# Kernel optimization log

Measured on AMD Instinct MI355X. Metric: run time of the kernel, lower is better.

## Reference

```python
import jax, jax.numpy as jnp
import numpy as np

B, S, D, H = 2, 2048, 1024, 16
HD = D // H
EPS = 1e-5


def setup_inputs() -> dict:
    key = jax.random.key(0)
    ks = jax.random.split(key, 12)
    s = 1.0 / np.sqrt(D)
    inp = {
        "q": jax.random.normal(ks[0], (B, S, D), jnp.float32),
        "k": jax.random.normal(ks[1], (B, S, D), jnp.float32),
        "v": jax.random.normal(ks[2], (B, S, D), jnp.float32),
        "mask": jnp.ones((B, S, S), jnp.int32),
        "Wq": jax.random.normal(ks[3], (D, D), jnp.float32) * s,
        "bq": jnp.zeros((D,), jnp.float32),
        "Wk": jax.random.normal(ks[4], (D, D), jnp.float32) * s,
        "bk": jnp.zeros((D,), jnp.float32),
        "Wv": jax.random.normal(ks[5], (D, D), jnp.float32) * s,
        "bv": jnp.zeros((D,), jnp.float32),
        "Wo": jax.random.normal(ks[6], (D, D), jnp.float32) * s,
        "bo": jnp.zeros((D,), jnp.float32),
        "gamma": jnp.ones((D,), jnp.float32),
        "beta": jnp.zeros((D,), jnp.float32),
    }
    return inp


def reference(q, k, v, mask, Wq, bq, Wk, bk, Wv, bv, Wo, bo, gamma, beta):
    residual = q
    # projections (torch Linear: x @ W.T + b)
    qh = (q @ Wq.T + bq).reshape(B, S, H, HD).transpose(0, 2, 1, 3)  # b h s d
    kh = (k @ Wk.T + bk).reshape(B, S, H, HD).transpose(0, 2, 1, 3)
    vh = (v @ Wv.T + bv).reshape(B, S, H, HD).transpose(0, 2, 1, 3)
    scores = jnp.einsum('bhid,bhjd->bhij', qh, kh) / jnp.sqrt(jnp.float32(HD))
    scores = jnp.where(mask[:, None, :, :] == 0, jnp.float32(-1e9), scores)
    attention = jax.nn.softmax(scores, axis=-1)  # dropout=0 (eval)
    context = jnp.einsum('bhij,bhjd->bhid', attention, vh)
    context = context.transpose(0, 2, 1, 3).reshape(B, S, D)
    out = context @ Wo.T + bo
    x = out + residual
    mu = jnp.mean(x, axis=-1, keepdims=True)
    var = jnp.mean(jnp.square(x - mu), axis=-1, keepdims=True)
    output = (x - mu) * jax.lax.rsqrt(var + EPS) * gamma + beta
    return (output, attention)
```

## Files before the change

### kernel.cpp

```cpp
#include <hip/hip_runtime.h>
#include <hip/hip_bf16.h>


typedef float f32x4 __attribute__((ext_vector_type(4)));
typedef short short8 __attribute__((ext_vector_type(8)));

#if __has_builtin(__builtin_amdgcn_exp2f)
#define EXP2(x) __builtin_amdgcn_exp2f(x)
#else
#define EXP2(x) exp2f(x)
#endif

#define QSCALE 0.18033688011112042f
#define MASKNEG -1.4426950408889634e9f

#define BAR_DRAIN8()  asm volatile("s_waitcnt vmcnt(8) lgkmcnt(0)\ns_barrier" ::: "memory")
#define BAR_LGKM()    asm volatile("s_waitcnt lgkmcnt(0)\ns_barrier" ::: "memory")

__device__ __forceinline__ short f2bs(float f) {
  union { __hip_bfloat16 h; short s; } u;
  u.h = __float2bfloat16(f);
  return u.s;
}

__device__ __forceinline__ void async16(const void* g, void* l) {
  __builtin_amdgcn_global_load_lds(
      (const __attribute__((address_space(1))) unsigned int*)g,
      (__attribute__((address_space(3))) unsigned int*)l, 16, 0, 0);
}

__global__ __launch_bounds__(256) void cvt_mask_kernel(
    const float* __restrict__ q, const float* __restrict__ k, const float* __restrict__ v,
    const float* __restrict__ wq, const float* __restrict__ wk, const float* __restrict__ wv,
    const float* __restrict__ wo, short* __restrict__ dst,
    const int* __restrict__ mask, unsigned* __restrict__ bits, unsigned* __restrict__ flags) {
  if (blockIdx.x < 8192) {
    long base = (long)blockIdx.x * 2048;
    const float* src;
    if      (base <  4194304) src = q  + base;
    else if (base <  8388608) src = k  + (base - 4194304);
    else if (base < 12582912) src = v  + (base - 8388608);
    else if (base < 13631488) src = wq + (base - 12582912);
    else if (base < 14680064) src = wk + (base - 13631488);
    else if (base < 15728640) src = wv + (base - 14680064);
    else                      src = wo + (base - 15728640);
    int off = threadIdx.x * 8;
    float4 a = *(const float4*)(src + off);
    float4 b = *(const float4*)(src + off + 4);
    short8 o;
    o[0] = f2bs(a.x); o[1] = f2bs(a.y); o[2] = f2bs(a.z); o[3] = f2bs(a.w);
    o[4] = f2bs(b.x); o[5] = f2bs(b.y); o[6] = f2bs(b.z); o[7] = f2bs(b.w);
    *(short8*)(dst + base + off) = o;
  } else {
    int bid = blockIdx.x - 8192;
    int t = threadIdx.x, w = t >> 6, lane = t & 63;
    for (int it = 0; it < 16; ++it) {
      long gw = (long)it * 8192 + bid * 4 + w;
      long base = gw * 64;
      int mv = mask[base + lane];
      unsigned long long m = __ballot(mv != 0);
      if (lane == 0)  bits[gw * 2]     = (unsigned)m;
      if (lane == 32) bits[gw * 2 + 1] = (unsigned)(m >> 32);
      if (lane == 0 && m != 0xFFFFFFFFFFFFFFFFull) {
        long j = base & 2047, i = (base >> 11) & 2047, b = base >> 22;
        atomicOr(&flags[(int)(b * 256 + (i >> 7) * 16 + (j >> 7))], 1u);
      }
    }
  }
}

__global__ __launch_bounds__(256, 2) void proj_kernel(
    const short* __restrict__ Abase, const short* __restrict__ Wbase,
    const float* __restrict__ bq, const float* __restrict__ bk, const float* __restrict__ bv,
    short* __restrict__ Qh, short* __restrict__ Kh, short* __restrict__ Vt) {
  __shared__ __align__(16) short As[2][128 * 64];
  __shared__ __align__(16) short Bs[2][128 * 64];
  const int mode = blockIdx.z;
  const short* A = Abase + (size_t)mode * 4194304;
  const short* W = Wbase + (size_t)mode * 1048576;
  const float* bias = (mode == 0) ? bq : (mode == 1 ? bk : bv);
  const int t = threadIdx.x, w = t >> 6, lane = t & 63, g = lane >> 4, lc = lane & 15;
  const int wrow = (w >> 1) * 64, wcol = (w & 1) * 64;
  const int m0 = blockIdx.x * 128, n0 = blockIdx.y * 128;

#define PSTAGE(buf, k0)                                                                     \
  do {                                                                                      \
    _Pragma("unroll") for (int i_ = 0; i_ < 4; i_++) {                                      \
      int cb = i_ * 256 + w * 64, ch = cb + lane, row = ch >> 3, c = ch & 7;                \
      int so = ((c ^ (row & 7)) << 3);                                                      \
      async16(A + (size_t)(m0 + row) * 1024 + (k0) + so, (void*)&As[buf][cb << 3]);         \
      async16(W + (size_t)(n0 + row) * 1024 + (k0) + so, (void*)&Bs[buf][cb << 3]);         \
    }                                                                                       \
  } while (0)

  f32x4 acc[4][4] = {};
  PSTAGE(0, 0);
  __syncthreads();
  int pb = 0;
  for (int kt = 0; kt < 16; ++kt) {
    if (kt < 15) PSTAGE(pb ^ 1, (kt + 1) * 64);
#pragma unroll
    for (int kf = 0; kf < 2; ++kf) {
      short8 af[4], bf[4];
#pragma unroll
      for (int m = 0; m < 4; m++) {
        int row = wrow + m * 16 + lc;
        af[m] = *(const short8*)&As[pb][(row << 6) + (((kf * 4 + g) ^ (row & 7)) << 3)];
      }
#pragma unroll
      for (int n = 0; n < 4; n++) {
        int row = wcol + n * 16 + lc;
        bf[n] = *(const short8*)&Bs[pb][(row << 6) + (((kf * 4 + g) ^ (row & 7)) << 3)];
      }
      __builtin_amdgcn_s_setprio(1);
#pragma unroll
      for (int m = 0; m < 4; m++)
#pragma unroll
        for (int n = 0; n < 4; n++)
          acc[m][n] = __builtin_amdgcn_mfma_f32_16x16x32_bf16(af[m], bf[n], acc[m][n], 0, 0, 0);
      __builtin_amdgcn_s_setprio(0);
    }
    __syncthreads();
    pb ^= 1;
  }
#undef PSTAGE
#pragma unroll
  for (int n = 0; n < 4; n++) {
    const int col = n0 + wcol + n * 16 + lc;
    const float bv_ = bias[col];
    const int h = col >> 6, d = col & 63;
#pragma unroll
    for (int m = 0; m < 4; m++)
#pragma unroll
      for (int r = 0; r < 4; r++) {
        const int srow = m0 + wrow + m * 16 + g * 4 + r;
        const int b = srow >> 11, s = srow & 2047;
        float val = acc[m][n][r] + bv_;
        if (mode == 0)
          Qh[((size_t)(b * 16 + h) * 2048 + s) * 64 + d] = f2bs(val * QSCALE);
        else if (mode == 1)
          Kh[((size_t)(b * 16 + h) * 2048 + s) * 64 + d] = f2bs(val);
        else
          Vt[((size_t)(b * 16 + h) * 64 + d) * 2048 + s] = f2bs(val);
      }
  }
}

__global__ __launch_bounds__(512, 4) void attn_kernel(
    const short* __restrict__ Qh, const short* __restrict__ Kh, const short* __restrict__ Vt,
    const unsigned* __restrict__ mbits, const unsigned* __restrict__ mflags,
    float* __restrict__ Pout, short* __restrict__ ctx) {
  __shared__ __align__(16) short Ks[2][128 * 64];
  __shared__ __align__(16) short Vs[64 * 128];
  __shared__ __align__(16) short Ps[128 * 128];
  const int L = blockIdx.x;
  const int xcd = L & 7, idx = L >> 3;
  const int bh = xcd + ((idx >> 4) << 3);
  const int qb = idx & 15;
  const int b = bh >> 4, h = bh & 15;
  const int t = threadIdx.x, w = t >> 6, lane = t & 63, g = lane >> 4, lc = lane & 15;
  const short* Qp = Qh + (size_t)bh * 2048 * 64;
  const short* Kp = Kh + (size_t)bh * 2048 * 64;
  const short* Vp = Vt + (size_t)bh * 64 * 2048;
  float* Pb = Pout + ((size_t)bh * 2048 + qb * 128) * 2048;

  short8 qf[2];
#pragma unroll
  for (int kf = 0; kf < 2; kf++)
    qf[kf] = *(const short8*)(Qp + (size_t)(qb * 128 + w * 16 + lc) * 64 + kf * 32 + g * 8);

#define STAGE_K(buf, j0)                                                                   \
  do {                                                                                     \
    _Pragma("unroll") for (int i_ = 0; i_ < 2; i_++) {                                     \
      int cb = i_ * 512 + w * 64, ch = cb + lane, row = ch >> 3, c = ch & 7;               \
      int sc = c ^ (row & 7) ^ ((row >> 3) & 7);                                           \
      async16(Kp + (size_t)((j0) + row) * 64 + (sc << 3), (void*)&Ks[buf][cb << 3]);       \
    }                                                                                      \
  } while (0)
#define STAGE_V(j0)                                                                        \
  do {                                                                                     \
    _Pragma("unroll") for (int i_ = 0; i_ < 2; i_++) {                                     \
      int cb = i_ * 512 + w * 64, ch = cb + lane, row = ch >> 4, c = ch & 15;              \
      async16(Vp + (size_t)row * 2048 + (j0) + ((c ^ (row & 15)) << 3), (void*)&Vs[cb << 3]); \
    }                                                                                      \
  } while (0)

  float lsum = 0.f;
  int kb = 0;
  STAGE_K(0, 0);
  __syncthreads();
  for (int it = 0; it < 16; ++it) {
    if (it < 15) STAGE_K(kb ^ 1, (it + 1) * 128);
    f32x4 acc[8] = {};
    __builtin_amdgcn_s_setprio(1);
#pragma unroll
    for (int kf = 0; kf < 2; kf++)
#pragma unroll
      for (int n = 0; n < 8; n++) {
        int row = n * 16 + lc;
        int sc = (kf * 4 + g) ^ (row & 7) ^ ((row >> 3) & 7);
        short8 kfr = *(const short8*)&Ks[kb][(row << 6) + (sc << 3)];
        acc[n] = __builtin_amdgcn_mfma_f32_16x16x32_bf16(kfr, qf[kf], acc[n], 0, 0, 0);
      }
    __builtin_amdgcn_s_setprio(0);
    unsigned flg = mflags[b * 256 + qb * 16 + it];
    if (flg) {
      int ig = qb * 128 + w * 16 + lc;
      uint4 mw = *(const uint4*)(mbits + ((size_t)b * 2048 + ig) * 64 + it * 4);
#pragma unroll
      for (int n = 0; n < 8; n++) {
        unsigned bw = (n >> 1) == 0 ? mw.x : ((n >> 1) == 1 ? mw.y : ((n >> 1) == 2 ? mw.z : mw.w));
#pragma unroll
        for (int r = 0; r < 4; r++)
          if (!((bw >> (((n & 1) << 4) + g * 4 + r)) & 1u)) acc[n][r] = MASKNEG;
      }
    }
    float s_ = 0.f;
#pragma unroll
    for (int n = 0; n < 8; n++)
#pragma unroll
      for (int r = 0; r < 4; r++) s_ += EXP2(acc[n][r]);
    s_ += __shfl_xor(s_, 16);
    s_ += __shfl_xor(s_, 32);
    lsum += s_;
    __syncthreads();
    kb ^= 1;
  }
  float* ls = (float*)Vs;
  if (g == 0) ls[w * 16 + lc] = lsum;
  __syncthreads();
  float linv[4];
#pragma unroll
  for (int r = 0; r < 4; r++) linv[r] = 1.0f / ls[w * 16 + g * 4 + r];
  kb = 0;
  STAGE_K(0, 0);
  __syncthreads();

  f32x4 acco[4] = {};
  for (int it = 0; it < 16; ++it) {
    const int j0 = it * 128;
    STAGE_V(j0);
    if (it < 15) STAGE_K(kb ^ 1, j0 + 128);
    f32x4 accs[8] = {};
    __builtin_amdgcn_s_setprio(1);
#pragma unroll
    for (int kf = 0; kf < 2; kf++)
#pragma unroll
      for (int n = 0; n < 8; n++) {
        int row = lc * 8 + n;
        int sc = (kf * 4 + g) ^ n ^ (lc & 7);
        short8 kfr = *(const short8*)&Ks[kb][(row << 6) + (sc << 3)];
        accs[n] = __builtin_amdgcn_mfma_f32_16x16x32_bf16(qf[kf], kfr, accs[n], 0, 0, 0);
      }
    __builtin_amdgcn_s_setprio(0);
    unsigned flg = mflags[b * 256 + qb * 16 + it];
    if (flg) {
#pragma unroll
      for (int r = 0; r < 4; r++) {
        int ig = qb * 128 + w * 16 + g * 4 + r;
        uint4 mw = *(const uint4*)(mbits + ((size_t)b * 2048 + ig) * 64 + it * 4);
        unsigned w01 = (lc & 4) ? mw.y : mw.x;
        unsigned w23 = (lc & 4) ? mw.w : mw.z;
        unsigned wsel = (lc & 8) ? w23 : w01;
#pragma unroll
        for (int n = 0; n < 8; n++)
          if (!((wsel >> (((lc & 3) << 3) + n)) & 1u)) accs[n][r] = MASKNEG;
      }
    }
#pragma unroll
    for (int r = 0; r < 4; r++) {
      const float li = linv[r];
      const int irow = w * 16 + g * 4 + r;
      f32x4 p0, p1;
#pragma unroll
      for (int n = 0; n < 4; n++) p0[n] = EXP2(accs[n][r]) * li;
#pragma unroll
      for (int n = 0; n < 4; n++) p1[n] = EXP2(accs[n + 4][r]) * li;
      float* pr = Pb + (size_t)irow * 2048 + j0 + (lc << 3);
      *(f32x4*)pr = p0;
      *(f32x4*)(pr + 4) = p1;
      short8 pk;
#pragma unroll
      for (int n = 0; n < 4; n++) { pk[n] = f2bs(p0[n]); pk[n + 4] = f2bs(p1[n]); }
      *(short8*)&Ps[(irow << 7) + ((lc ^ (irow & 15)) << 3)] = pk;
    }
    BAR_DRAIN8();
    __builtin_amdgcn_s_setprio(1);
#pragma unroll
    for (int kt4 = 0; kt4 < 4; kt4++) {
      int prow = w * 16 + lc;
      short8 pa = *(const short8*)&Ps[(prow << 7) + ((((kt4 << 2) + g) ^ (prow & 15)) << 3)];
#pragma unroll
      for (int dn = 0; dn < 4; dn++) {
        int d = dn * 16 + lc;
        short8 vb_ = *(const short8*)&Vs[(d << 7) + ((((kt4 << 2) + g) ^ (d & 15)) << 3)];
        acco[dn] = __builtin_amdgcn_mfma_f32_16x16x32_bf16(pa, vb_, acco[dn], 0, 0, 0);
      }
    }
    __builtin_amdgcn_s_setprio(0);
    BAR_LGKM();
    kb ^= 1;
  }
#pragma unroll
  for (int dn = 0; dn < 4; dn++)
#pragma unroll
    for (int r = 0; r < 4; r++) {
      int srow = qb * 128 + w * 16 + g * 4 + r;
      int col = h * 64 + dn * 16 + lc;
      ctx[(size_t)(b * 2048 + srow) * 1024 + col] = f2bs(acco[dn][r]);
    }
#undef STAGE_K
#undef STAGE_V
}

__global__ __launch_bounds__(256, 2) void oproj_kernel(
    const short* __restrict__ A, const short* __restrict__ W,
    const float* __restrict__ bo, const float* __restrict__ qres, float* __restrict__ xo) {
  __shared__ __align__(16) short As[2][128 * 64];
  __shared__ __align__(16) short Bs[2][128 * 64];
  const int t = threadIdx.x, w = t >> 6, lane = t & 63, g = lane >> 4, lc = lane & 15;
  const int wrow = (w >> 1) * 64, wcol = (w & 1) * 64;
  const int m0 = blockIdx.x * 128, n0 = blockIdx.y * 128;

#define OSTAGE(buf, k0)                                                                     \
  do {                                                                                      \
    _Pragma("unroll") for (int i_ = 0; i_ < 4; i_++) {                                      \
      int cb = i_ * 256 + w * 64, ch = cb + lane, row = ch >> 3, c = ch & 7;                \
      int so = ((c ^ (row & 7)) << 3);                                                      \
      async16(A + (size_t)(m0 + row) * 1024 + (k0) + so, (void*)&As[buf][cb << 3]);         \
      async16(W + (size_t)(n0 + row) * 1024 + (k0) + so, (void*)&Bs[buf][cb << 3]);         \
    }                                                                                       \
  } while (0)

  f32x4 acc[4][4] = {};
  OSTAGE(0, 0);
  __syncthreads();
  int pb = 0;
  for (int kt = 0; kt < 16; ++kt) {
    if (kt < 15) OSTAGE(pb ^ 1, (kt + 1) * 64);
#pragma unroll
    for (int kf = 0; kf < 2; ++kf) {
      short8 af[4], bf[4];
#pragma unroll
      for (int m = 0; m < 4; m++) {
        int row = wrow + m * 16 + lc;
        af[m] = *(const short8*)&As[pb][(row << 6) + (((kf * 4 + g) ^ (row & 7)) << 3)];
      }
#pragma unroll
      for (int n = 0; n < 4; n++) {
        int row = wcol + n * 16 + lc;
        bf[n] = *(const short8*)&Bs[pb][(row << 6) + (((kf * 4 + g) ^ (row & 7)) << 3)];
      }
      __builtin_amdgcn_s_setprio(1);
#pragma unroll
      for (int m = 0; m < 4; m++)
#pragma unroll
        for (int n = 0; n < 4; n++)
          acc[m][n] = __builtin_amdgcn_mfma_f32_16x16x32_bf16(af[m], bf[n], acc[m][n], 0, 0, 0);
      __builtin_amdgcn_s_setprio(0);
    }
    __syncthreads();
    pb ^= 1;
  }
#undef OSTAGE
#pragma unroll
  for (int n = 0; n < 4; n++) {
    const int col = n0 + wcol + n * 16 + lc;
    const float bv_ = bo[col];
#pragma unroll
    for (int m = 0; m < 4; m++)
#pragma unroll
      for (int r = 0; r < 4; r++) {
        const int srow = m0 + wrow + m * 16 + g * 4 + r;
        size_t o = (size_t)srow * 1024 + col;
        xo[o] = acc[m][n][r] + bv_ + qres[o];
      }
  }
}

__global__ __launch_bounds__(256) void ln_kernel(const float* __restrict__ x,
                                                 const float* __restrict__ gamma,
                                                 const float* __restrict__ beta,
                                                 float* __restrict__ out) {
  const int row = blockIdx.x, t = threadIdx.x;
  const float4 v = ((const float4*)(x + (size_t)row * 1024))[t];
  float s = v.x + v.y + v.z + v.w;
  float sq = v.x * v.x + v.y * v.y + v.z * v.z + v.w * v.w;
#pragma unroll
  for (int off = 1; off < 64; off <<= 1) { s += __shfl_xor(s, off); sq += __shfl_xor(sq, off); }
  __shared__ float ss[4], sqs[4];
  const int w = t >> 6, lane = t & 63;
  if (lane == 0) { ss[w] = s; sqs[w] = sq; }
  __syncthreads();
  s = ss[0] + ss[1] + ss[2] + ss[3];
  sq = sqs[0] + sqs[1] + sqs[2] + sqs[3];
  const float mu = s * (1.f / 1024.f);
  const float var = sq * (1.f / 1024.f) - mu * mu;
  const float rs = rsqrtf(var + 1e-5f);
  const float4 gm = ((const float4*)gamma)[t];
  const float4 bt = ((const float4*)beta)[t];
  float4 o;
  o.x = (v.x - mu) * rs * gm.x + bt.x;
  o.y = (v.y - mu) * rs * gm.y + bt.y;
  o.z = (v.z - mu) * rs * gm.z + bt.z;
  o.w = (v.w - mu) * rs * gm.w + bt.w;
  ((float4*)(out + (size_t)row * 1024))[t] = o;
}

extern "C" void kernel_launch(void* const* d_in, const int* in_sizes, int n_in,
                              void* d_out, int out_size, void* d_ws, size_t ws_size,
                              hipStream_t stream) {
  (void)in_sizes; (void)n_in; (void)out_size; (void)ws_size;
  const float* q     = (const float*)d_in[0];
  const float* k     = (const float*)d_in[1];
  const float* v     = (const float*)d_in[2];
  const int*   mask  = (const int*)d_in[3];
  const float* Wq    = (const float*)d_in[4];
  const float* bq    = (const float*)d_in[5];
  const float* Wk    = (const float*)d_in[6];
  const float* bk    = (const float*)d_in[7];
  const float* Wv    = (const float*)d_in[8];
  const float* bv    = (const float*)d_in[9];
  const float* Wo    = (const float*)d_in[10];
  const float* bo    = (const float*)d_in[11];
  const float* gamma = (const float*)d_in[12];
  const float* beta  = (const float*)d_in[13];

  char* ws = (char*)d_ws;
  short* cvtdst = (short*)ws;
  short* Qh     = (short*)(ws + 33554432);
  short* Kh     = (short*)(ws + 41943040);
  short* Vt     = (short*)(ws + 50331648);
  unsigned* mbits  = (unsigned*)(ws + 58720256);
  unsigned* mflags = (unsigned*)(ws + 59768832);
  float* x   = (float*)ws;
  short* ctx = (short*)(ws + 16777216);

  float* outln = (float*)d_out;
  float* Pout  = (float*)d_out + 4194304;

  hipMemsetAsync(mflags, 0, 2048, stream);
  cvt_mask_kernel<<<10240, 256, 0, stream>>>(q, k, v, Wq, Wk, Wv, Wo, cvtdst, mask, mbits, mflags);
  proj_kernel<<<dim3(32, 8, 3), 256, 0, stream>>>(cvtdst, cvtdst + 12582912, bq, bk, bv, Qh, Kh, Vt);
  attn_kernel<<<512, 512, 0, stream>>>(Qh, Kh, Vt, mbits, mflags, Pout, ctx);
  oproj_kernel<<<dim3(32, 8), 256, 0, stream>>>(ctx, cvtdst + 15728640, bo, q, x);
  ln_kernel<<<4096, 256, 0, stream>>>(x, gamma, beta, outln);
}
```

Measured before the change: 285.3 us.

## Deepen K prefetch in attention row-sum pass with five-slot LDS ring

Merges the attention kernel's separate K, V and P shared buffers into one five-slot LDS array. The first pass, which computes the softmax row sums, now prefetches two K tiles ahead and handles two tiles per barrier pair, cutting barriers and exposing less load latency. The second pass changes its vmcnt waits so the prefetched K load can stay in flight past the P-V barrier. This adds fragile hand-counted waitcnt values, and an error in those counts would cause races.

```diff
diff --git a/kernel.cpp b/kernel.cpp
--- a/kernel.cpp
+++ b/kernel.cpp
@@ -13,9 +13,6 @@
 
 #define QSCALE 0.18033688011112042f
 #define MASKNEG -1.4426950408889634e9f
-
-#define BAR_DRAIN8()  asm volatile("s_waitcnt vmcnt(8) lgkmcnt(0)\ns_barrier" ::: "memory")
-#define BAR_LGKM()    asm volatile("s_waitcnt lgkmcnt(0)\ns_barrier" ::: "memory")
 
 __device__ __forceinline__ short f2bs(float f) {
   union { __hip_bfloat16 h; short s; } u;
@@ -150,9 +147,7 @@
     const short* __restrict__ Qh, const short* __restrict__ Kh, const short* __restrict__ Vt,
     const unsigned* __restrict__ mbits, const unsigned* __restrict__ mflags,
     float* __restrict__ Pout, short* __restrict__ ctx) {
-  __shared__ __align__(16) short Ks[2][128 * 64];
-  __shared__ __align__(16) short Vs[64 * 128];
-  __shared__ __align__(16) short Ps[128 * 128];
+  __shared__ __align__(16) short SH[5][8192];
   const int L = blockIdx.x;
   const int xcd = L & 7, idx = L >> 3;
   const int bh = xcd + ((idx >> 4) << 3);
@@ -169,78 +164,88 @@
   for (int kf = 0; kf < 2; kf++)
     qf[kf] = *(const short8*)(Qp + (size_t)(qb * 128 + w * 16 + lc) * 64 + kf * 32 + g * 8);
 
-#define STAGE_K(buf, j0)                                                                   \
+#define STAGE_KS(dst, tj)                                                                  \
   do {                                                                                     \
     _Pragma("unroll") for (int i_ = 0; i_ < 2; i_++) {                                     \
       int cb = i_ * 512 + w * 64, ch = cb + lane, row = ch >> 3, c = ch & 7;               \
       int sc = c ^ (row & 7) ^ ((row >> 3) & 7);                                           \
-      async16(Kp + (size_t)((j0) + row) * 64 + (sc << 3), (void*)&Ks[buf][cb << 3]);       \
+      async16(Kp + (size_t)((tj) * 128 + row) * 64 + (sc << 3), (void*)&(dst)[cb << 3]);   \
     }                                                                                      \
   } while (0)
 #define STAGE_V(j0)                                                                        \
   do {                                                                                     \
     _Pragma("unroll") for (int i_ = 0; i_ < 2; i_++) {                                     \
       int cb = i_ * 512 + w * 64, ch = cb + lane, row = ch >> 4, c = ch & 15;              \
-      async16(Vp + (size_t)row * 2048 + (j0) + ((c ^ (row & 15)) << 3), (void*)&Vs[cb << 3]); \
+      async16(Vp + (size_t)row * 2048 + (j0) + ((c ^ (row & 15)) << 3), (void*)&SH[2][cb << 3]); \
     }                                                                                      \
   } while (0)
 
   float lsum = 0.f;
+  STAGE_KS((&SH[0][0]), 0);
+  STAGE_KS((&SH[1][0]), 1);
+  for (int p = 0; p < 8; ++p) {
+    asm volatile("s_waitcnt lgkmcnt(0)\ns_barrier" ::: "memory");
+    if (p < 7) {
+      STAGE_KS((&SH[(2 * p + 2) % 5][0]), 2 * p + 2);
+      STAGE_KS((&SH[(2 * p + 3) % 5][0]), 2 * p + 3);
+    }
+    if (p < 7) asm volatile("s_waitcnt vmcnt(4)\ns_barrier" ::: "memory");
+    else       asm volatile("s_waitcnt vmcnt(0)\ns_barrier" ::: "memory");
+#pragma unroll
+    for (int half = 0; half < 2; ++half) {
+      const int it = 2 * p + half;
+      const short* Kslot = &SH[it % 5][0];
+      f32x4 acc[8] = {};
+      __builtin_amdgcn_s_setprio(1);
+#pragma unroll
+      for (int kf = 0; kf < 2; kf++)
+#pragma unroll
+        for (int n = 0; n < 8; n++) {
+          int row = n * 16 + lc;
+          int sc = (kf * 4 + g) ^ (row & 7) ^ ((row >> 3) & 7);
+          short8 kfr = *(const short8*)&Kslot[(row << 6) + (sc << 3)];
+          acc[n] = __builtin_amdgcn_mfma_f32_16x16x32_bf16(kfr, qf[kf], acc[n], 0, 0, 0);
+        }
+      __builtin_amdgcn_s_setprio(0);
+      unsigned flg = mflags[b * 256 + qb * 16 + it];
+      if (flg) {
+        int ig = qb * 128 + w * 16 + lc;
+        uint4 mw = *(const uint4*)(mbits + ((size_t)b * 2048 + ig) * 64 + it * 4);
+#pragma unroll
+        for (int n = 0; n < 8; n++) {
+          unsigned bw = (n >> 1) == 0 ? mw.x : ((n >> 1) == 1 ? mw.y : ((n >> 1) == 2 ? mw.z : mw.w));
+#pragma unroll
+          for (int r = 0; r < 4; r++)
+            if (!((bw >> (((n & 1) << 4) + g * 4 + r)) & 1u)) acc[n][r] = MASKNEG;
+        }
+      }
+      float s_ = 0.f;
+#pragma unroll
+      for (int n = 0; n < 8; n++)
+#pragma unroll
+        for (int r = 0; r < 4; r++) s_ += EXP2(acc[n][r]);
+      s_ += __shfl_xor(s_, 16);
+      s_ += __shfl_xor(s_, 32);
+      lsum += s_;
+    }
+  }
+  float* ls = (float*)&SH[2][0];
+  __syncthreads();
+  if (g == 0) ls[w * 16 + lc] = lsum;
+  __syncthreads();
+  float linv[4];
+#pragma unroll
+  for (int r = 0; r < 4; r++) linv[r] = 1.0f / ls[w * 16 + g * 4 + r];
+  STAGE_KS((&SH[0][0]), 0);
+  __syncthreads();
+
+  short* Ps = &SH[3][0];
+  f32x4 acco[4] = {};
   int kb = 0;
-  STAGE_K(0, 0);
-  __syncthreads();
-  for (int it = 0; it < 16; ++it) {
-    if (it < 15) STAGE_K(kb ^ 1, (it + 1) * 128);
-    f32x4 acc[8] = {};
-    __builtin_amdgcn_s_setprio(1);
-#pragma unroll
-    for (int kf = 0; kf < 2; kf++)
-#pragma unroll
-      for (int n = 0; n < 8; n++) {
-        int row = n * 16 + lc;
-        int sc = (kf * 4 + g) ^ (row & 7) ^ ((row >> 3) & 7);
-        short8 kfr = *(const short8*)&Ks[kb][(row << 6) + (sc << 3)];
-        acc[n] = __builtin_amdgcn_mfma_f32_16x16x32_bf16(kfr, qf[kf], acc[n], 0, 0, 0);
-      }
-    __builtin_amdgcn_s_setprio(0);
-    unsigned flg = mflags[b * 256 + qb * 16 + it];
-    if (flg) {
-      int ig = qb * 128 + w * 16 + lc;
-      uint4 mw = *(const uint4*)(mbits + ((size_t)b * 2048 + ig) * 64 + it * 4);
-#pragma unroll
-      for (int n = 0; n < 8; n++) {
-        unsigned bw = (n >> 1) == 0 ? mw.x : ((n >> 1) == 1 ? mw.y : ((n >> 1) == 2 ? mw.z : mw.w));
-#pragma unroll
-        for (int r = 0; r < 4; r++)
-          if (!((bw >> (((n & 1) << 4) + g * 4 + r)) & 1u)) acc[n][r] = MASKNEG;
-      }
-    }
-    float s_ = 0.f;
-#pragma unroll
-    for (int n = 0; n < 8; n++)
-#pragma unroll
-      for (int r = 0; r < 4; r++) s_ += EXP2(acc[n][r]);
-    s_ += __shfl_xor(s_, 16);
-    s_ += __shfl_xor(s_, 32);
-    lsum += s_;
-    __syncthreads();
-    kb ^= 1;
-  }
-  float* ls = (float*)Vs;
-  if (g == 0) ls[w * 16 + lc] = lsum;
-  __syncthreads();
-  float linv[4];
-#pragma unroll
-  for (int r = 0; r < 4; r++) linv[r] = 1.0f / ls[w * 16 + g * 4 + r];
-  kb = 0;
-  STAGE_K(0, 0);
-  __syncthreads();
-
-  f32x4 acco[4] = {};
   for (int it = 0; it < 16; ++it) {
     const int j0 = it * 128;
     STAGE_V(j0);
-    if (it < 15) STAGE_K(kb ^ 1, j0 + 128);
+    if (it < 15) STAGE_KS((&SH[kb ^ 1][0]), it + 1);
     f32x4 accs[8] = {};
     __builtin_amdgcn_s_setprio(1);
 #pragma unroll
@@ -249,7 +254,7 @@
       for (int n = 0; n < 8; n++) {
         int row = lc * 8 + n;
         int sc = (kf * 4 + g) ^ n ^ (lc & 7);
-        short8 kfr = *(const short8*)&Ks[kb][(row << 6) + (sc << 3)];
+        short8 kfr = *(const short8*)&SH[kb][(row << 6) + (sc << 3)];
         accs[n] = __builtin_amdgcn_mfma_f32_16x16x32_bf16(qf[kf], kfr, accs[n], 0, 0, 0);
       }
     __builtin_amdgcn_s_setprio(0);
@@ -284,7 +289,8 @@
       for (int n = 0; n < 4; n++) { pk[n] = f2bs(p0[n]); pk[n + 4] = f2bs(p1[n]); }
       *(short8*)&Ps[(irow << 7) + ((lc ^ (irow & 15)) << 3)] = pk;
     }
-    BAR_DRAIN8();
+    if (it < 15) asm volatile("s_waitcnt vmcnt(10) lgkmcnt(0)\ns_barrier" ::: "memory");
+    else         asm volatile("s_waitcnt vmcnt(8) lgkmcnt(0)\ns_barrier" ::: "memory");
     __builtin_amdgcn_s_setprio(1);
 #pragma unroll
     for (int kt4 = 0; kt4 < 4; kt4++) {
@@ -293,12 +299,12 @@
 #pragma unroll
       for (int dn = 0; dn < 4; dn++) {
         int d = dn * 16 + lc;
-        short8 vb_ = *(const short8*)&Vs[(d << 7) + ((((kt4 << 2) + g) ^ (d & 15)) << 3)];
+        short8 vb_ = *(const short8*)&SH[2][(d << 7) + ((((kt4 << 2) + g) ^ (d & 15)) << 3)];
         acco[dn] = __builtin_amdgcn_mfma_f32_16x16x32_bf16(pa, vb_, acco[dn], 0, 0, 0);
       }
     }
     __builtin_amdgcn_s_setprio(0);
-    BAR_LGKM();
+    asm volatile("s_waitcnt vmcnt(8) lgkmcnt(0)\ns_barrier" ::: "memory");
     kb ^= 1;
   }
 #pragma unroll
@@ -309,7 +315,7 @@
       int col = h * 64 + dn * 16 + lc;
       ctx[(size_t)(b * 2048 + srow) * 1024 + col] = f2bs(acco[dn][r]);
     }
-#undef STAGE_K
+#undef STAGE_KS
 #undef STAGE_V
 }
 
```

Result: slower. 310.8 us (+8.9%).
